# Kernel optimization log

Hardware: AMD Instinct MI355X
Metric: run time of the kernel (lower is better)

The kernel has to match this reference:

```python
import jax, jax.numpy as jnp
import numpy as np

B, L, D, DK, T = 8192, 64, 512, 64, 128
WIDE_IN = 2 * T + T * T  # 16640


def setup_inputs() -> dict:
    key = jax.random.key(0)
    ks = jax.random.split(key, 24)
    s = 0.02
    inp = {
        "mashup_tags": jax.random.uniform(ks[0], (B, T), jnp.float32),
        "target_api_tags": jax.random.uniform(ks[1], (B, T), jnp.float32),
        "cross_product_tag": jax.random.uniform(ks[2], (B, T * T), jnp.float32),
        "encoded_api_context": jax.random.normal(ks[3], (B, L, D), jnp.float32),
        "candidate_api_description_feature": jax.random.normal(ks[4], (B, D), jnp.float32),
        "mashup_description_feature": jax.random.normal(ks[5], (B, D), jnp.float32),
        "context_len": jax.random.randint(ks[6], (B,), 0, L + 1, jnp.int64 if jax.config.jax_enable_x64 else jnp.int32),
        # attention projections (torch Linear weight layout: [out, in], no bias)
        "W_K": s * jax.random.normal(ks[7], (DK, D), jnp.float32),
        "W_Q": s * jax.random.normal(ks[8], (DK, D), jnp.float32),
        # wide head
        "wide_w": s * jax.random.normal(ks[9], (1, WIDE_IN), jnp.float32),
        "wide_b": jnp.zeros((1,), jnp.float32),
        # deep MLP 1536->512->256->128->1
        "d1_w": s * jax.random.normal(ks[10], (512, 3 * D), jnp.float32),
        "d1_b": jnp.zeros((512,), jnp.float32),
        "d2_w": s * jax.random.normal(ks[11], (256, 512), jnp.float32),
        "d2_b": jnp.zeros((256,), jnp.float32),
        "d3_w": s * jax.random.normal(ks[12], (128, 256), jnp.float32),
        "d3_b": jnp.zeros((128,), jnp.float32),
        "d4_w": s * jax.random.normal(ks[13], (1, 128), jnp.float32),
        "d4_b": jnp.zeros((1,), jnp.float32),
        "wide_weight": jnp.ones((1,), jnp.float32),
        "deep_weight": jnp.ones((1,), jnp.float32),
        "bias": jnp.zeros((1,), jnp.float32),
    }
    return inp


def reference(mashup_tags, target_api_tags, cross_product_tag,
              encoded_api_context, candidate_api_description_feature,
              mashup_description_feature, context_len,
              W_K, W_Q, wide_w, wide_b,
              d1_w, d1_b, d2_w, d2_b, d3_w, d3_b, d4_w, d4_b,
              wide_weight, deep_weight, bias):
    # ---- wide branch ----
    wide_in = jnp.concatenate([mashup_tags, target_api_tags, cross_product_tag], axis=1)
    wide_out = jax.nn.sigmoid(wide_in @ wide_w.T + wide_b)  # (B,1)

    # ---- ragged attention (vectorized masked softmax replaces the Python batch loop) ----
    K = jnp.einsum("bld,kd->blk", encoded_api_context, W_K)          # (B,L,dk)
    Q = candidate_api_description_feature @ W_Q.T                     # (B,dk)
    scores = jnp.einsum("blk,bk->bl", K, Q)                           # (B,L)
    mask = jnp.arange(scores.shape[1])[None, :] < context_len[:, None]
    m = jnp.max(jnp.where(mask, scores, -1e30), axis=-1, keepdims=True)
    e = jnp.where(mask, jnp.exp(scores - m), 0.0)
    denom = jnp.sum(e, axis=-1, keepdims=True)
    probs = e / jnp.maximum(denom, 1e-30)  # rows with length==0 -> all zeros (matches torch zeros fallback)
    api_context = jnp.einsum("bl,bld->bd", probs, encoded_api_context)  # (B,512)

    # ---- deep branch ----
    deep_in = jnp.concatenate([mashup_description_feature, api_context,
                               candidate_api_description_feature], axis=1)  # (B,1536)
    h = jax.nn.relu(deep_in @ d1_w.T + d1_b)
    h = jax.nn.relu(h @ d2_w.T + d2_b)
    h = jax.nn.relu(h @ d3_w.T + d3_b)
    deep_out = h @ d4_w.T + d4_b  # (B,1)

    out = wide_weight * wide_out + deep_weight * deep_out + bias
    return jax.nn.sigmoid(out)
```

## Files before the change

kernel.cpp:

```cpp
#include <hip/hip_runtime.h>

#define Bsz 8192
#define Lctx 64
#define Ddim 512
#define DK 64
#define Ttag 128
#define RQT 2

using f32x4 = __attribute__((ext_vector_type(4))) float;
using bf16x8 = __attribute__((ext_vector_type(8))) short;

__device__ __forceinline__ float wave_sum(float v) {
#pragma unroll
    for (int m = 32; m > 0; m >>= 1) v += __shfl_xor(v, m, 64);
    return v;
}

__device__ __forceinline__ float wave_max(float v) {
#pragma unroll
    for (int m = 32; m > 0; m >>= 1) v = fmaxf(v, __shfl_xor(v, m, 64));
    return v;
}

__device__ __forceinline__ float dot4(float4 a, float4 b) {
    return a.x * b.x + a.y * b.y + a.z * b.z + a.w * b.w;
}

__device__ __forceinline__ unsigned f2bf(float f) {
    unsigned int u = __float_as_uint(f);
    u = u + 0x7fffu + ((u >> 16) & 1u);
    return u >> 16;
}
__device__ __forceinline__ unsigned pack2(float a, float b) {
    return f2bf(a) | (f2bf(b) << 16);
}
__device__ __forceinline__ float bf2f(unsigned short u) { return __uint_as_float((unsigned)u << 16); }

__global__ __launch_bounds__(256) void k_f2bf3(
    const float* __restrict__ s1, unsigned short* __restrict__ d1,
    const float* __restrict__ s2, unsigned short* __restrict__ d2,
    const float* __restrict__ s3, unsigned short* __restrict__ d3)
{
    int i = blockIdx.x * 256 + threadIdx.x;
    const float* s;
    unsigned short* d;
    if (i < 196608)      { s = s1; d = d1; }
    else if (i < 229376) { i -= 196608; s = s2; d = d2; }
    else if (i < 237568) { i -= 229376; s = s3; d = d3; }
    else return;
    const float4 v = ((const float4*)s)[i];
    uint2 w;
    w.x = pack2(v.x, v.y);
    w.y = pack2(v.z, v.w);
    *(uint2*)&d[(size_t)i * 4] = w;
}

__global__ __launch_bounds__(256) void k_qtilde(
    const float* __restrict__ C, const float* __restrict__ WQ,
    const float* __restrict__ WK, float* __restrict__ qt)
{
    const int lane = threadIdx.x & 63;
    const int gw = blockIdx.x * 4 + (threadIdx.x >> 6);
    const int b0 = gw * RQT;

    float4 c0[RQT], c1[RQT];
#pragma unroll
    for (int r = 0; r < RQT; ++r) {
        const float4* row = (const float4*)(C + (size_t)(b0 + r) * Ddim);
        c0[r] = row[lane];
        c1[r] = row[64 + lane];
    }
    float tv[RQT];
#pragma unroll
    for (int r = 0; r < RQT; ++r) tv[r] = 0.f;
    for (int k = 0; k < DK; ++k) {
        const float4* wrow = (const float4*)(WQ + (size_t)k * Ddim);
        const float4 w0 = wrow[lane];
        const float4 w1 = wrow[64 + lane];
#pragma unroll
        for (int r = 0; r < RQT; ++r) {
            float p = dot4(c0[r], w0) + dot4(c1[r], w1);
            p = wave_sum(p);
            if (lane == k) tv[r] = p;
        }
    }
    float4 a0[RQT], a1[RQT];
#pragma unroll
    for (int r = 0; r < RQT; ++r) {
        a0[r] = make_float4(0.f, 0.f, 0.f, 0.f);
        a1[r] = make_float4(0.f, 0.f, 0.f, 0.f);
    }
    for (int k = 0; k < DK; ++k) {
        const float4* wrow = (const float4*)(WK + (size_t)k * Ddim);
        const float4 w0 = wrow[lane];
        const float4 w1 = wrow[64 + lane];
#pragma unroll
        for (int r = 0; r < RQT; ++r) {
            const float tk = __shfl(tv[r], k, 64);
            a0[r].x += tk * w0.x; a0[r].y += tk * w0.y;
            a0[r].z += tk * w0.z; a0[r].w += tk * w0.w;
            a1[r].x += tk * w1.x; a1[r].y += tk * w1.y;
            a1[r].z += tk * w1.z; a1[r].w += tk * w1.w;
        }
    }
#pragma unroll
    for (int r = 0; r < RQT; ++r) {
        float4* orow = (float4*)(qt + (size_t)(b0 + r) * Ddim);
        orow[lane] = a0[r];
        orow[64 + lane] = a1[r];
    }
}

__global__ __launch_bounds__(256, 8) void k_attn_wide(
    const float* __restrict__ X, const float* __restrict__ qt,
    const int* __restrict__ clen, const float* __restrict__ mdesc,
    const float* __restrict__ cand,
    const float* __restrict__ mt, const float* __restrict__ tt,
    const float* __restrict__ cp, const float* __restrict__ ww,
    const float* __restrict__ wb,
    unsigned short* __restrict__ din, float* __restrict__ wl)
{
    __shared__ float sl[Lctx];
    __shared__ float part[4][Ddim];
    __shared__ float Mw[4];
    __shared__ float red[4];
    __shared__ float MD[2];

    const int b = blockIdx.x;
    const int tid = threadIdx.x;
    const int wave = tid >> 6, lane = tid & 63;
    const int len = clen[b];
    const int nrw = (len > wave) ? ((len - wave + 3) >> 2) : 0;

    const float4* xb = (const float4*)(X + (size_t)b * Lctx * Ddim);

    float4 y0 = make_float4(0.f, 0.f, 0.f, 0.f);
    float4 y1 = make_float4(0.f, 0.f, 0.f, 0.f);
    float mw = -1e30f;

    if (nrw > 0) {
        const float4* qrow = (const float4*)(qt + (size_t)b * Ddim);
        const float4 q0 = qrow[lane];
        const float4 q1 = qrow[64 + lane];
        for (int k = 0; k < nrw; k += 2) {
            const int l0 = wave + k * 4;
            const int l1 = wave + min(k + 1, nrw - 1) * 4;
            const float4 a0 = xb[l0 * 128 + lane];
            const float4 a1 = xb[l0 * 128 + 64 + lane];
            const float4 c0 = xb[l1 * 128 + lane];
            const float4 c1 = xb[l1 * 128 + 64 + lane];
            float s0 = dot4(a0, q0) + dot4(a1, q1);
            float s1 = dot4(c0, q0) + dot4(c1, q1);
            s0 = wave_sum(s0);
            s1 = wave_sum(s1);
            const bool has1 = (k + 1 < nrw);
            if (lane == 0) {
                sl[l0] = s0;
                if (has1) sl[l1] = s1;
            }
            const float pm = has1 ? fmaxf(s0, s1) : s0;
            const float mn = fmaxf(mw, pm);
            const float scale = __expf(mw - mn);
            const float e0 = __expf(s0 - mn);
            const float e1 = has1 ? __expf(s1 - mn) : 0.f;
            y0.x = y0.x * scale + e0 * a0.x + e1 * c0.x;
            y0.y = y0.y * scale + e0 * a0.y + e1 * c0.y;
            y0.z = y0.z * scale + e0 * a0.z + e1 * c0.z;
            y0.w = y0.w * scale + e0 * a0.w + e1 * c0.w;
            y1.x = y1.x * scale + e0 * a1.x + e1 * c1.x;
            y1.y = y1.y * scale + e0 * a1.y + e1 * c1.y;
            y1.z = y1.z * scale + e0 * a1.z + e1 * c1.z;
            y1.w = y1.w * scale + e0 * a1.w + e1 * c1.w;
            mw = mn;
        }
    }
    *(float4*)&part[wave][lane * 4] = y0;
    *(float4*)&part[wave][256 + lane * 4] = y1;
    if (lane == 0) Mw[wave] = mw;

    float wacc = 0.f;
    if (tid < 64) {
        float4 v;
        if (tid < 32) v = ((const float4*)(mt + (size_t)b * Ttag))[tid];
        else          v = ((const float4*)(tt + (size_t)b * Ttag))[tid - 32];
        wacc += dot4(v, ((const float4*)ww)[tid]);
    }
    {
        const float4* cp4 = (const float4*)(cp + (size_t)b * (Ttag * Ttag));
        const float4* ww4 = (const float4*)(ww + 2 * Ttag);
#pragma unroll 2
        for (int i = tid; i < (Ttag * Ttag) / 4; i += 256)
            wacc += dot4(cp4[i], ww4[i]);
    }
    wacc = wave_sum(wacc);
    if (lane == 0) red[wave] = wacc;

    const float4 mv = (tid < 128)
        ? ((const float4*)(mdesc + (size_t)b * Ddim))[tid]
        : ((const float4*)(cand + (size_t)b * Ddim))[tid - 128];

    __syncthreads();

    if (wave == 0) {
        const float s = (lane < len) ? sl[lane] : -1e30f;
        const float m = wave_max(s);
        const float e = (lane < len) ? __expf(s - m) : 0.f;
        const float d = wave_sum(e);
        if (lane == 0) {
            MD[0] = m;
            MD[1] = 1.f / fmaxf(d, 1e-30f);
        }
    }
    __syncthreads();

    const float Mg = MD[0], rD = MD[1];
    const float f0 = __expf(Mw[0] - Mg) * rD;
    const float f1 = __expf(Mw[1] - Mg) * rD;
    const float f2 = __expf(Mw[2] - Mg) * rD;
    const float f3 = __expf(Mw[3] - Mg) * rD;

    unsigned short* dr = din + (size_t)b * 1536;
    {
        const int d0 = tid * 2;
        const float2 p0 = *(const float2*)&part[0][d0];
        const float2 p1 = *(const float2*)&part[1][d0];
        const float2 p2 = *(const float2*)&part[2][d0];
        const float2 p3 = *(const float2*)&part[3][d0];
        const float vx = p0.x * f0 + p1.x * f1 + p2.x * f2 + p3.x * f3;
        const float vy = p0.y * f0 + p1.y * f1 + p2.y * f2 + p3.y * f3;
        *(unsigned*)&dr[512 + d0] = pack2(vx, vy);
    }
    {
        uint2 w;
        w.x = pack2(mv.x, mv.y);
        w.y = pack2(mv.z, mv.w);
        const int off = (tid < 128) ? tid * 4 : 1024 + (tid - 128) * 4;
        *(uint2*)&dr[off] = w;
    }
    if (tid == 0) wl[b] = red[0] + red[1] + red[2] + red[3] + wb[0];
}

__global__ __launch_bounds__(256) void k_gemm_bf16(
    const unsigned short* __restrict__ A, const unsigned short* __restrict__ W,
    const float* __restrict__ bias, unsigned short* __restrict__ C,
    const int K, const int N, const int relu)
{
    __shared__ unsigned short As[128][72];
    __shared__ unsigned short Bs[128][72];
    const int tid = threadIdx.x;
    const int wave = tid >> 6, lane = tid & 63;
    const int wm = wave >> 1, wn = wave & 1;
    const size_t m0 = (size_t)blockIdx.x * 128;
    const size_t n0 = (size_t)blockIdx.y * 128;

    f32x4 acc[4][4];
#pragma unroll
    for (int i = 0; i < 4; ++i)
#pragma unroll
        for (int j = 0; j < 4; ++j) acc[i][j] = (f32x4){0.f, 0.f, 0.f, 0.f};

    uint4 pa[4], pb[4];
    auto loadA = [&](int k0) {
#pragma unroll
        for (int j = 0; j < 4; ++j) {
            const int i = tid + j * 256;
            const int row = i >> 3, c8 = (i & 7) * 8;
            pa[j] = *(const uint4*)(A + (m0 + row) * (size_t)K + k0 + c8);
        }
    };
    auto loadB = [&](int k0) {
#pragma unroll
        for (int j = 0; j < 4; ++j) {
            const int i = tid + j * 256;
            const int row = i >> 3, c8 = (i & 7) * 8;
            pb[j] = *(const uint4*)(W + (n0 + row) * (size_t)K + k0 + c8);
        }
    };

    loadA(0);
    loadB(0);
    for (int k0 = 0; k0 < K; k0 += 64) {
        __syncthreads();
#pragma unroll
        for (int j = 0; j < 4; ++j) {
            const int i = tid + j * 256;
            const int row = i >> 3, c8 = (i & 7) * 8;
            *(uint4*)&As[row][c8] = pa[j];
            *(uint4*)&Bs[row][c8] = pb[j];
        }
        __syncthreads();
        if (k0 + 64 < K) { loadA(k0 + 64); loadB(k0 + 64); }
#pragma unroll
        for (int kk = 0; kk < 2; ++kk) {
            const int krow = kk * 32 + (lane >> 4) * 8;
            bf16x8 af[4], bfr[4];
#pragma unroll
            for (int mm = 0; mm < 4; ++mm)
                af[mm] = *(const bf16x8*)&As[wm * 64 + mm * 16 + (lane & 15)][krow];
#pragma unroll
            for (int nn = 0; nn < 4; ++nn)
                bfr[nn] = *(const bf16x8*)&Bs[wn * 64 + nn * 16 + (lane & 15)][krow];
#pragma unroll
            for (int mm = 0; mm < 4; ++mm)
#pragma unroll
                for (int nn = 0; nn < 4; ++nn)
                    acc[mm][nn] = __builtin_amdgcn_mfma_f32_16x16x32_bf16(
                        af[mm], bfr[nn], acc[mm][nn], 0, 0, 0);
        }
    }

#pragma unroll
    for (int nn = 0; nn < 4; ++nn) {
        const int col = (int)n0 + wn * 64 + nn * 16 + (lane & 15);
        const float bv = bias[col];
#pragma unroll
        for (int mm = 0; mm < 4; ++mm) {
#pragma unroll
            for (int r = 0; r < 4; ++r) {
                const size_t row = m0 + wm * 64 + mm * 16 + (lane >> 4) * 4 + r;
                float v = acc[mm][nn][r] + bv;
                if (relu) v = fmaxf(v, 0.f);
                C[row * N + col] = (unsigned short)f2bf(v);
            }
        }
    }
}

__global__ __launch_bounds__(256) void k_final(
    const unsigned short* __restrict__ h3, const float* __restrict__ d4w,
    const float* __restrict__ d4b, const float* __restrict__ wl,
    const float* __restrict__ wwt, const float* __restrict__ dwt,
    const float* __restrict__ bs, float* __restrict__ out)
{
    const int lane = threadIdx.x & 63;
    const int b = blockIdx.x * 4 + (threadIdx.x >> 6);
    const unsigned short* hr = h3 + (size_t)b * 128;
    float v = bf2f(hr[lane]) * d4w[lane] + bf2f(hr[64 + lane]) * d4w[64 + lane];
    v = wave_sum(v);
    if (lane == 0) {
        const float deep = v + d4b[0];
        const float wo = 1.f / (1.f + __expf(-wl[b]));
        const float z = wwt[0] * wo + dwt[0] * deep + bs[0];
        out[b] = 1.f / (1.f + __expf(-z));
    }
}

extern "C" void kernel_launch(void* const* d_in, const int* in_sizes, int n_in,
                              void* d_out, int out_size, void* d_ws, size_t ws_size,
                              hipStream_t stream)
{
    const float* mt    = (const float*)d_in[0];
    const float* tt    = (const float*)d_in[1];
    const float* cp    = (const float*)d_in[2];
    const float* X     = (const float*)d_in[3];
    const float* cand  = (const float*)d_in[4];
    const float* mdesc = (const float*)d_in[5];
    const int*   clen  = (const int*)d_in[6];
    const float* WK    = (const float*)d_in[7];
    const float* WQ    = (const float*)d_in[8];
    const float* ww    = (const float*)d_in[9];
    const float* wb    = (const float*)d_in[10];
    const float* d1w   = (const float*)d_in[11];
    const float* d1b   = (const float*)d_in[12];
    const float* d2w   = (const float*)d_in[13];
    const float* d2b   = (const float*)d_in[14];
    const float* d3w   = (const float*)d_in[15];
    const float* d3b   = (const float*)d_in[16];
    const float* d4w   = (const float*)d_in[17];
    const float* d4b   = (const float*)d_in[18];
    const float* wwt   = (const float*)d_in[19];
    const float* dwt   = (const float*)d_in[20];
    const float* bs    = (const float*)d_in[21];
    float* out = (float*)d_out;

    char* w = (char*)d_ws;
    unsigned short* din = (unsigned short*)w;            w += (size_t)Bsz * 1536 * 2;
    float* qt           = (float*)w;                     w += (size_t)Bsz * 512 * 4;
    unsigned short* h1  = (unsigned short*)w;            w += (size_t)Bsz * 512 * 2;
    unsigned short* h2  = (unsigned short*)w;            w += (size_t)Bsz * 256 * 2;
    unsigned short* h3  = (unsigned short*)w;            w += (size_t)Bsz * 128 * 2;
    float* wl           = (float*)w;                     w += (size_t)Bsz * 4;
    unsigned short* w1b = (unsigned short*)w;            w += (size_t)512 * 1536 * 2;
    unsigned short* w2b = (unsigned short*)w;            w += (size_t)256 * 512 * 2;
    unsigned short* w3b = (unsigned short*)w;            w += (size_t)128 * 256 * 2;

    hipLaunchKernelGGL(k_f2bf3, dim3(928), dim3(256), 0, stream,
                       d1w, w1b, d2w, w2b, d3w, w3b);
    hipLaunchKernelGGL(k_qtilde, dim3(Bsz / (RQT * 4)), dim3(256), 0, stream,
                       cand, WQ, WK, qt);
    hipLaunchKernelGGL(k_attn_wide, dim3(Bsz), dim3(256), 0, stream,
                       X, qt, clen, mdesc, cand, mt, tt, cp, ww, wb, din, wl);
    hipLaunchKernelGGL(k_gemm_bf16, dim3(64, 4), dim3(256), 0, stream,
                       din, w1b, d1b, h1, 1536, 512, 1);
    hipLaunchKernelGGL(k_gemm_bf16, dim3(64, 2), dim3(256), 0, stream,
                       h1, w2b, d2b, h2, 512, 256, 1);
    hipLaunchKernelGGL(k_gemm_bf16, dim3(64, 1), dim3(256), 0, stream,
                       h2, w3b, d3b, h3, 256, 128, 1);
    hipLaunchKernelGGL(k_final, dim3(Bsz / 4), dim3(256), 0, stream,
                       h3, d4w, d4b, wl, wwt, dwt, bs, out);
}
```

Baseline: 406.8 us.

## Fuse deep MLP layers 2-4 with final sigmoid and merge prep kernels

Merges the weight bf16 conversion and the q-tilde projection into one launch. Fuses GEMM layers 2 and 3, the final 128->1 dot and the sigmoid combine into a single kernel that keeps h2 in shared memory, so the h2/h3 global round trips and two launches go away. The first GEMM is templated and uses 64x128 tiles, giving 512 blocks instead of 256 for better CU occupancy. The fused kernel launches only 128 blocks, each holding a large shared-memory footprint, so its parallelism on the GPU is limited.

New measurement: 416.9 us. 1.02x slower.

```diff
diff --git a/kernel.cpp b/kernel.cpp
--- a/kernel.cpp
+++ b/kernel.cpp
@@ -34,31 +34,29 @@
 __device__ __forceinline__ unsigned pack2(float a, float b) {
     return f2bf(a) | (f2bf(b) << 16);
 }
-__device__ __forceinline__ float bf2f(unsigned short u) { return __uint_as_float((unsigned)u << 16); }
-
-__global__ __launch_bounds__(256) void k_f2bf3(
+
+__global__ __launch_bounds__(256) void k_prep(
+    const float* __restrict__ C, const float* __restrict__ WQ,
+    const float* __restrict__ WK, float* __restrict__ qt,
     const float* __restrict__ s1, unsigned short* __restrict__ d1,
     const float* __restrict__ s2, unsigned short* __restrict__ d2,
     const float* __restrict__ s3, unsigned short* __restrict__ d3)
 {
-    int i = blockIdx.x * 256 + threadIdx.x;
-    const float* s;
-    unsigned short* d;
-    if (i < 196608)      { s = s1; d = d1; }
-    else if (i < 229376) { i -= 196608; s = s2; d = d2; }
-    else if (i < 237568) { i -= 229376; s = s3; d = d3; }
-    else return;
-    const float4 v = ((const float4*)s)[i];
-    uint2 w;
-    w.x = pack2(v.x, v.y);
-    w.y = pack2(v.z, v.w);
-    *(uint2*)&d[(size_t)i * 4] = w;
-}
-
-__global__ __launch_bounds__(256) void k_qtilde(
-    const float* __restrict__ C, const float* __restrict__ WQ,
-    const float* __restrict__ WK, float* __restrict__ qt)
-{
+    if (blockIdx.x >= 1024) {
+        int i = (blockIdx.x - 1024) * 256 + threadIdx.x;
+        const float* s;
+        unsigned short* d;
+        if (i < 196608)      { s = s1; d = d1; }
+        else if (i < 229376) { i -= 196608; s = s2; d = d2; }
+        else                 { i -= 229376; s = s3; d = d3; }
+        const float4 v = ((const float4*)s)[i];
+        uint2 w;
+        w.x = pack2(v.x, v.y);
+        w.y = pack2(v.z, v.w);
+        *(uint2*)&d[(size_t)i * 4] = w;
+        return;
+    }
+
     const int lane = threadIdx.x & 63;
     const int gw = blockIdx.x * 4 + (threadIdx.x >> 6);
     const int b0 = gw * RQT;
@@ -240,29 +238,34 @@
     if (tid == 0) wl[b] = red[0] + red[1] + red[2] + red[3] + wb[0];
 }
 
+template <int BM, int BN>
 __global__ __launch_bounds__(256) void k_gemm_bf16(
     const unsigned short* __restrict__ A, const unsigned short* __restrict__ W,
     const float* __restrict__ bias, unsigned short* __restrict__ C,
     const int K, const int N, const int relu)
 {
-    __shared__ unsigned short As[128][72];
-    __shared__ unsigned short Bs[128][72];
+    constexpr int WM = BM / 2, WN = BN / 2;
+    constexpr int MM = WM / 16, NN = WN / 16;
+    constexpr int NA = (BM * 8) / 256;
+    constexpr int NB = (BN * 8) / 256;
+    __shared__ unsigned short As[BM][72];
+    __shared__ unsigned short Bs[BN][72];
     const int tid = threadIdx.x;
     const int wave = tid >> 6, lane = tid & 63;
     const int wm = wave >> 1, wn = wave & 1;
-    const size_t m0 = (size_t)blockIdx.x * 128;
-    const size_t n0 = (size_t)blockIdx.y * 128;
-
-    f32x4 acc[4][4];
-#pragma unroll
-    for (int i = 0; i < 4; ++i)
-#pragma unroll
-        for (int j = 0; j < 4; ++j) acc[i][j] = (f32x4){0.f, 0.f, 0.f, 0.f};
-
-    uint4 pa[4], pb[4];
+    const size_t m0 = (size_t)blockIdx.x * BM;
+    const size_t n0 = (size_t)blockIdx.y * BN;
+
+    f32x4 acc[MM][NN];
+#pragma unroll
+    for (int i = 0; i < MM; ++i)
+#pragma unroll
+        for (int j = 0; j < NN; ++j) acc[i][j] = (f32x4){0.f, 0.f, 0.f, 0.f};
+
+    uint4 pa[NA], pb[NB];
     auto loadA = [&](int k0) {
 #pragma unroll
-        for (int j = 0; j < 4; ++j) {
+        for (int j = 0; j < NA; ++j) {
             const int i = tid + j * 256;
             const int row = i >> 3, c8 = (i & 7) * 8;
             pa[j] = *(const uint4*)(A + (m0 + row) * (size_t)K + k0 + c8);
@@ -270,7 +273,7 @@
     };
     auto loadB = [&](int k0) {
 #pragma unroll
-        for (int j = 0; j < 4; ++j) {
+        for (int j = 0; j < NB; ++j) {
             const int i = tid + j * 256;
             const int row = i >> 3, c8 = (i & 7) * 8;
             pb[j] = *(const uint4*)(W + (n0 + row) * (size_t)K + k0 + c8);
@@ -282,10 +285,15 @@
     for (int k0 = 0; k0 < K; k0 += 64) {
         __syncthreads();
 #pragma unroll
-        for (int j = 0; j < 4; ++j) {
+        for (int j = 0; j < NA; ++j) {
             const int i = tid + j * 256;
             const int row = i >> 3, c8 = (i & 7) * 8;
             *(uint4*)&As[row][c8] = pa[j];
+        }
+#pragma unroll
+        for (int j = 0; j < NB; ++j) {
+            const int i = tid + j * 256;
+            const int row = i >> 3, c8 = (i & 7) * 8;
             *(uint4*)&Bs[row][c8] = pb[j];
         }
         __syncthreads();
@@ -293,31 +301,31 @@
 #pragma unroll
         for (int kk = 0; kk < 2; ++kk) {
             const int krow = kk * 32 + (lane >> 4) * 8;
-            bf16x8 af[4], bfr[4];
-#pragma unroll
-            for (int mm = 0; mm < 4; ++mm)
-                af[mm] = *(const bf16x8*)&As[wm * 64 + mm * 16 + (lane & 15)][krow];
-#pragma unroll
-            for (int nn = 0; nn < 4; ++nn)
-                bfr[nn] = *(const bf16x8*)&Bs[wn * 64 + nn * 16 + (lane & 15)][krow];
-#pragma unroll
-            for (int mm = 0; mm < 4; ++mm)
-#pragma unroll
-                for (int nn = 0; nn < 4; ++nn)
+            bf16x8 af[MM], bfr[NN];
+#pragma unroll
+            for (int mm = 0; mm < MM; ++mm)
+                af[mm] = *(const bf16x8*)&As[wm * WM + mm * 16 + (lane & 15)][krow];
+#pragma unroll
+            for (int nn = 0; nn < NN; ++nn)
+                bfr[nn] = *(const bf16x8*)&Bs[wn * WN + nn * 16 + (lane & 15)][krow];
+#pragma unroll
+            for (int mm = 0; mm < MM; ++mm)
+#pragma unroll
+                for (int nn = 0; nn < NN; ++nn)
                     acc[mm][nn] = __builtin_amdgcn_mfma_f32_16x16x32_bf16(
                         af[mm], bfr[nn], acc[mm][nn], 0, 0, 0);
         }
     }
 
 #pragma unroll
-    for (int nn = 0; nn < 4; ++nn) {
-        const int col = (int)n0 + wn * 64 + nn * 16 + (lane & 15);
+    for (int nn = 0; nn < NN; ++nn) {
+        const int col = (int)n0 + wn * WN + nn * 16 + (lane & 15);
         const float bv = bias[col];
 #pragma unroll
-        for (int mm = 0; mm < 4; ++mm) {
+        for (int mm = 0; mm < MM; ++mm) {
 #pragma unroll
             for (int r = 0; r < 4; ++r) {
-                const size_t row = m0 + wm * 64 + mm * 16 + (lane >> 4) * 4 + r;
+                const size_t row = m0 + wm * WM + mm * 16 + (lane >> 4) * 4 + r;
                 float v = acc[mm][nn][r] + bv;
                 if (relu) v = fmaxf(v, 0.f);
                 C[row * N + col] = (unsigned short)f2bf(v);
@@ -326,19 +334,164 @@
     }
 }
 
-__global__ __launch_bounds__(256) void k_final(
-    const unsigned short* __restrict__ h3, const float* __restrict__ d4w,
+__global__ __launch_bounds__(256) void k_gemm23f(
+    const unsigned short* __restrict__ h1, const unsigned short* __restrict__ w2,
+    const float* __restrict__ b2, const unsigned short* __restrict__ w3,
+    const float* __restrict__ b3, const float* __restrict__ d4w,
     const float* __restrict__ d4b, const float* __restrict__ wl,
     const float* __restrict__ wwt, const float* __restrict__ dwt,
     const float* __restrict__ bs, float* __restrict__ out)
 {
-    const int lane = threadIdx.x & 63;
-    const int b = blockIdx.x * 4 + (threadIdx.x >> 6);
-    const unsigned short* hr = h3 + (size_t)b * 128;
-    float v = bf2f(hr[lane]) * d4w[lane] + bf2f(hr[64 + lane]) * d4w[64 + lane];
-    v = wave_sum(v);
-    if (lane == 0) {
-        const float deep = v + d4b[0];
+    __shared__ unsigned short As[64][72];
+    __shared__ unsigned short Bs[256][72];
+    __shared__ unsigned short h2l[64][264];
+    __shared__ float dp[64][2];
+    const int tid = threadIdx.x;
+    const int wave = tid >> 6, lane = tid & 63;
+    const int wm = wave >> 1, wn = wave & 1;
+    const size_t m0 = (size_t)blockIdx.x * 64;
+
+    f32x4 acc[2][8];
+#pragma unroll
+    for (int i = 0; i < 2; ++i)
+#pragma unroll
+        for (int j = 0; j < 8; ++j) acc[i][j] = (f32x4){0.f, 0.f, 0.f, 0.f};
+
+    uint4 pa[2], pb[8];
+    auto loadA = [&](int k0) {
+#pragma unroll
+        for (int j = 0; j < 2; ++j) {
+            const int i = tid + j * 256;
+            const int row = i >> 3, c8 = (i & 7) * 8;
+            pa[j] = *(const uint4*)(h1 + (m0 + row) * 512 + k0 + c8);
+        }
+    };
+    auto loadB = [&](int k0) {
+#pragma unroll
+        for (int j = 0; j < 8; ++j) {
+            const int i = tid + j * 256;
+            const int row = i >> 3, c8 = (i & 7) * 8;
+            pb[j] = *(const uint4*)(w2 + (size_t)row * 512 + k0 + c8);
+        }
+    };
+
+    loadA(0);
+    loadB(0);
+    for (int k0 = 0; k0 < 512; k0 += 64) {
+        __syncthreads();
+#pragma unroll
+        for (int j = 0; j < 2; ++j) {
+            const int i = tid + j * 256;
+            const int row = i >> 3, c8 = (i & 7) * 8;
+            *(uint4*)&As[row][c8] = pa[j];
+        }
+#pragma unroll
+        for (int j = 0; j < 8; ++j) {
+            const int i = tid + j * 256;
+            const int row = i >> 3, c8 = (i & 7) * 8;
+            *(uint4*)&Bs[row][c8] = pb[j];
+        }
+        __syncthreads();
+        if (k0 + 64 < 512) { loadA(k0 + 64); loadB(k0 + 64); }
+#pragma unroll
+        for (int kk = 0; kk < 2; ++kk) {
+            const int krow = kk * 32 + (lane >> 4) * 8;
+            bf16x8 af[2], bfr[8];
+#pragma unroll
+            for (int mm = 0; mm < 2; ++mm)
+                af[mm] = *(const bf16x8*)&As[wm * 32 + mm * 16 + (lane & 15)][krow];
+#pragma unroll
+            for (int nn = 0; nn < 8; ++nn)
+                bfr[nn] = *(const bf16x8*)&Bs[wn * 128 + nn * 16 + (lane & 15)][krow];
+#pragma unroll
+            for (int mm = 0; mm < 2; ++mm)
+#pragma unroll
+                for (int nn = 0; nn < 8; ++nn)
+                    acc[mm][nn] = __builtin_amdgcn_mfma_f32_16x16x32_bf16(
+                        af[mm], bfr[nn], acc[mm][nn], 0, 0, 0);
+        }
+    }
+#pragma unroll
+    for (int nn = 0; nn < 8; ++nn) {
+        const int col = wn * 128 + nn * 16 + (lane & 15);
+        const float bv = b2[col];
+#pragma unroll
+        for (int mm = 0; mm < 2; ++mm) {
+#pragma unroll
+            for (int r = 0; r < 4; ++r) {
+                const int row = wm * 32 + mm * 16 + (lane >> 4) * 4 + r;
+                h2l[row][col] = (unsigned short)f2bf(fmaxf(acc[mm][nn][r] + bv, 0.f));
+            }
+        }
+    }
+    __syncthreads();
+
+    f32x4 acc2[2][4];
+#pragma unroll
+    for (int i = 0; i < 2; ++i)
+#pragma unroll
+        for (int j = 0; j < 4; ++j) acc2[i][j] = (f32x4){0.f, 0.f, 0.f, 0.f};
+
+    for (int k0 = 0; k0 < 256; k0 += 64) {
+#pragma unroll
+        for (int j = 0; j < 4; ++j) {
+            const int i = tid + j * 256;
+            const int row = i >> 3, c8 = (i & 7) * 8;
+            *(uint4*)&Bs[row][c8] = *(const uint4*)(w3 + (size_t)row * 256 + k0 + c8);
+        }
+        __syncthreads();
+#pragma unroll
+        for (int kk = 0; kk < 2; ++kk) {
+            const int krow = kk * 32 + (lane >> 4) * 8;
+            bf16x8 af[2], bfr[4];
+#pragma unroll
+            for (int mm = 0; mm < 2; ++mm)
+                af[mm] = *(const bf16x8*)&h2l[wm * 32 + mm * 16 + (lane & 15)][k0 + krow];
+#pragma unroll
+            for (int nn = 0; nn < 4; ++nn)
+                bfr[nn] = *(const bf16x8*)&Bs[wn * 64 + nn * 16 + (lane & 15)][krow];
+#pragma unroll
+            for (int mm = 0; mm < 2; ++mm)
+#pragma unroll
+                for (int nn = 0; nn < 4; ++nn)
+                    acc2[mm][nn] = __builtin_amdgcn_mfma_f32_16x16x32_bf16(
+                        af[mm], bfr[nn], acc2[mm][nn], 0, 0, 0);
+        }
+        __syncthreads();
+    }
+
+    float rowpart[2][4];
+#pragma unroll
+    for (int mm = 0; mm < 2; ++mm)
+#pragma unroll
+        for (int r = 0; r < 4; ++r) rowpart[mm][r] = 0.f;
+#pragma unroll
+    for (int nn = 0; nn < 4; ++nn) {
+        const int col = wn * 64 + nn * 16 + (lane & 15);
+        const float bv = b3[col];
+        const float w4 = d4w[col];
+#pragma unroll
+        for (int mm = 0; mm < 2; ++mm)
+#pragma unroll
+            for (int r = 0; r < 4; ++r)
+                rowpart[mm][r] += fmaxf(acc2[mm][nn][r] + bv, 0.f) * w4;
+    }
+#pragma unroll
+    for (int mm = 0; mm < 2; ++mm)
+#pragma unroll
+        for (int r = 0; r < 4; ++r) {
+            float v = rowpart[mm][r];
+            v += __shfl_xor(v, 1, 64);
+            v += __shfl_xor(v, 2, 64);
+            v += __shfl_xor(v, 4, 64);
+            v += __shfl_xor(v, 8, 64);
+            if ((lane & 15) == 0)
+                dp[wm * 32 + mm * 16 + (lane >> 4) * 4 + r][wn] = v;
+        }
+    __syncthreads();
+    if (tid < 64) {
+        const float deep = dp[tid][0] + dp[tid][1] + d4b[0];
+        const size_t b = m0 + tid;
         const float wo = 1.f / (1.f + __expf(-wl[b]));
         const float z = wwt[0] * wo + dwt[0] * deep + bs[0];
         out[b] = 1.f / (1.f + __expf(-z));
@@ -377,25 +530,17 @@
     unsigned short* din = (unsigned short*)w;            w += (size_t)Bsz * 1536 * 2;
     float* qt           = (float*)w;                     w += (size_t)Bsz * 512 * 4;
     unsigned short* h1  = (unsigned short*)w;            w += (size_t)Bsz * 512 * 2;
-    unsigned short* h2  = (unsigned short*)w;            w += (size_t)Bsz * 256 * 2;
-    unsigned short* h3  = (unsigned short*)w;            w += (size_t)Bsz * 128 * 2;
     float* wl           = (float*)w;                     w += (size_t)Bsz * 4;
     unsigned short* w1b = (unsigned short*)w;            w += (size_t)512 * 1536 * 2;
     unsigned short* w2b = (unsigned short*)w;            w += (size_t)256 * 512 * 2;
     unsigned short* w3b = (unsigned short*)w;            w += (size_t)128 * 256 * 2;
 
-    hipLaunchKernelGGL(k_f2bf3, dim3(928), dim3(256), 0, stream,
-                       d1w, w1b, d2w, w2b, d3w, w3b);
-    hipLaunchKernelGGL(k_qtilde, dim3(Bsz / (RQT * 4)), dim3(256), 0, stream,
-                       cand, WQ, WK, qt);
+    hipLaunchKernelGGL(k_prep, dim3(1952), dim3(256), 0, stream,
+                       cand, WQ, WK, qt, d1w, w1b, d2w, w2b, d3w, w3b);
     hipLaunchKernelGGL(k_attn_wide, dim3(Bsz), dim3(256), 0, stream,
                        X, qt, clen, mdesc, cand, mt, tt, cp, ww, wb, din, wl);
-    hipLaunchKernelGGL(k_gemm_bf16, dim3(64, 4), dim3(256), 0, stream,
+    hipLaunchKernelGGL((k_gemm_bf16<64, 128>), dim3(128, 4), dim3(256), 0, stream,
                        din, w1b, d1b, h1, 1536, 512, 1);
-    hipLaunchKernelGGL(k_gemm_bf16, dim3(64, 2), dim3(256), 0, stream,
-                       h1, w2b, d2b, h2, 512, 256, 1);
-    hipLaunchKernelGGL(k_gemm_bf16, dim3(64, 1), dim3(256), 0, stream,
-                       h2, w3b, d3b, h3, 256, 128, 1);
-    hipLaunchKernelGGL(k_final, dim3(Bsz / 4), dim3(256), 0, stream,
-                       h3, d4w, d4b, wl, wwt, dwt, bs, out);
-}
+    hipLaunchKernelGGL(k_gemm23f, dim3(128), dim3(256), 0, stream,
+                       h1, w2b, d2b, w3b, d3b, d4w, d4b, wl, wwt, dwt, bs, out);
+}
```
